# Kernel optimization log

Measured on AMD Instinct MI355X. Metric: run time of the kernel, lower is better.

Reference implementation:

```python
import jax, jax.numpy as jnp
import numpy as np

HIDDEN = 4096
N_HEADS = 32
N_KV_HEADS = 8
D_HEAD = HIDDEN // N_HEADS  # 128
SEQ_LEN = 2048
ROPE_THETA = 10000.0


def _rope(t, start_index):
    # t: [L, n_heads, d_head]; rotate-half (Llama-style) RoPE
    L, _, d = t.shape
    inv_freq = 1.0 / (ROPE_THETA ** (jnp.arange(0, d, 2, dtype=jnp.float32) / d))  # [d/2]
    pos = jnp.arange(L, dtype=jnp.float32) + jnp.float32(start_index)  # [L]
    ang = pos[:, None] * inv_freq  # [L, d/2]
    cos = jnp.cos(ang)[:, None, :].astype(t.dtype)  # [L, 1, d/2]
    sin = jnp.sin(ang)[:, None, :].astype(t.dtype)
    t1, t2 = jnp.split(t, 2, axis=-1)
    return jnp.concatenate([t1 * cos - t2 * sin, t1 * sin + t2 * cos], axis=-1)


def setup_inputs() -> dict:
    key = jax.random.key(0)
    ks = jax.random.split(key, 5)
    s = 1.0 / np.sqrt(HIDDEN)
    return {
        "x": jax.random.normal(ks[0], (SEQ_LEN, HIDDEN), dtype=jnp.float32),
        "Wq": jax.random.normal(ks[1], (HIDDEN, N_HEADS * D_HEAD), dtype=jnp.float32) * s,
        "Wk": jax.random.normal(ks[2], (HIDDEN, N_KV_HEADS * D_HEAD), dtype=jnp.float32) * s,
        "Wv": jax.random.normal(ks[3], (HIDDEN, N_KV_HEADS * D_HEAD), dtype=jnp.float32) * s,
        "Wo": jax.random.normal(ks[4], (N_HEADS * D_HEAD, HIDDEN), dtype=jnp.float32) * s,
        "start_index": 0,
    }


def reference(x, Wq, Wk, Wv, Wo, start_index):
    # x: [L, hidden]; start_index==0 -> cache reset, so post-write cache == current k, v
    L, _ = x.shape
    q = (x @ Wq).reshape(L, N_HEADS, D_HEAD)
    k = (x @ Wk).reshape(L, N_KV_HEADS, D_HEAD)
    v = (x @ Wv).reshape(L, N_KV_HEADS, D_HEAD)
    q = _rope(q, start_index)
    k = _rope(k, start_index)
    # KV cache read: full cache is just [L] entries (prefill)
    S = L
    g = N_HEADS // N_KV_HEADS
    qh = q.transpose(1, 0, 2).reshape(N_KV_HEADS, g, L, D_HEAD)  # [kv, g, L, d]
    kh = k.transpose(1, 0, 2)  # [kv, S, d]
    vh = v.transpose(1, 0, 2)  # [kv, S, d]
    scale = 1.0 / np.sqrt(D_HEAD)
    scores = jnp.einsum('kgld,ksd->kgls', qh, kh) * jnp.asarray(scale, qh.dtype)
    # is_causal = (L > 1): tril(L, S) mask
    causal = jnp.tril(jnp.ones((L, S), dtype=bool))
    neg = jnp.asarray(jnp.finfo(scores.dtype).min, scores.dtype)
    scores = jnp.where(causal, scores, neg)
    attn = jax.nn.softmax(scores, axis=-1)
    out = jnp.einsum('kgls,ksd->kgld', attn, vh)  # [kv, g, L, d]
    out = out.reshape(N_HEADS, L, D_HEAD).transpose(1, 0, 2).reshape(L, N_HEADS * D_HEAD)
    return out @ Wo
```

## Files before the change

kernel.cpp:

```cpp
#include <hip/hip_runtime.h>

typedef unsigned short u16;
typedef float f32x4 __attribute__((ext_vector_type(4)));
typedef __bf16 bf16x8 __attribute__((ext_vector_type(8)));
typedef u16 u16x8 __attribute__((ext_vector_type(8)));

#define VMCNT(n) asm volatile("s_waitcnt vmcnt(" #n ")" ::: "memory")

static __device__ __forceinline__ u16 f2bf(float f) {
  union { float f; unsigned u; } v; v.f = f;
  unsigned r = v.u + 0x7fffu + ((v.u >> 16) & 1u);
  return (u16)(r >> 16);
}
static __device__ __forceinline__ u16 f2bf_n(float f) {
  __bf16 h = (__bf16)f;
  return __builtin_bit_cast(u16, h);
}
static __device__ __forceinline__ float bf2f(u16 x) {
  union { unsigned u; float f; } v; v.u = (unsigned)x << 16; return v.f;
}

static __device__ __forceinline__ f32x4 mfma16(u16x8 a, u16x8 b, f32x4 c) {
  return __builtin_amdgcn_mfma_f32_16x16x32_bf16(
      __builtin_bit_cast(bf16x8, a), __builtin_bit_cast(bf16x8, b), c, 0, 0, 0);
}

static __device__ __forceinline__ void load_lds16(const void* g, void* l) {
  __builtin_amdgcn_global_load_lds(
      (const __attribute__((address_space(1))) void*)g,
      (__attribute__((address_space(3))) void*)l, 16, 0, 0);
}

__global__ void cvt_f32_bf16_swz(const float* __restrict__ in, u16* __restrict__ out, int n8) {
  int i = blockIdx.x * blockDim.x + threadIdx.x;
  if (i >= n8) return;
  int row = i >> 9;
  int j = i & 511;
  int jp = (j & ~7) | ((j & 7) ^ (row & 7));
  const float* src = in + (size_t)i * 8;
  u16x8 o;
  #pragma unroll
  for (int e = 0; e < 8; e++) o[e] = f2bf(src[e]);
  *(u16x8*)(out + ((size_t)row << 12) + jp * 8) = o;
}

__global__ __launch_bounds__(256)
void transpose_cvt(const float* __restrict__ W, u16* __restrict__ Wt, int K, int N) {
  __shared__ float tile[128][33];
  const int k0 = blockIdx.x * 128, n0 = blockIdx.y * 32;
  const int tr = threadIdx.x >> 3;
  const int tc4 = (threadIdx.x & 7) * 4;
  #pragma unroll
  for (int it = 0; it < 4; it++) {
    int kl = it * 32 + tr;
    float4 v = *(const float4*)&W[(size_t)(k0 + kl) * N + n0 + tc4];
    tile[kl][tc4] = v.x; tile[kl][tc4 + 1] = v.y;
    tile[kl][tc4 + 2] = v.z; tile[kl][tc4 + 3] = v.w;
  }
  __syncthreads();
  const int nl = threadIdx.x >> 4;
  const int dch = threadIdx.x & 15;
  #pragma unroll
  for (int it = 0; it < 2; it++) {
    int n = n0 + it * 16 + nl;
    int sch = (dch & 8) | ((dch & 7) ^ (n & 7));
    u16x8 o;
    #pragma unroll
    for (int e = 0; e < 8; e++) o[e] = f2bf(tile[sch * 8 + e][it * 16 + nl]);
    *(u16x8*)&Wt[(size_t)n * K + k0 + dch * 8] = o;
  }
}

__global__ __launch_bounds__(256)
void transpose_cvt2(const float* __restrict__ Wk, const float* __restrict__ Wv,
                    u16* __restrict__ Wkt, u16* __restrict__ Wvt, int K, int N) {
  __shared__ float tile[128][33];
  const int sel = blockIdx.y >= (unsigned)(N / 32);
  const int n0 = (blockIdx.y - (sel ? N / 32 : 0)) * 32;
  const float* W = sel ? Wv : Wk;
  u16* Wt = sel ? Wvt : Wkt;
  const int k0 = blockIdx.x * 128;
  const int tr = threadIdx.x >> 3;
  const int tc4 = (threadIdx.x & 7) * 4;
  #pragma unroll
  for (int it = 0; it < 4; it++) {
    int kl = it * 32 + tr;
    float4 v = *(const float4*)&W[(size_t)(k0 + kl) * N + n0 + tc4];
    tile[kl][tc4] = v.x; tile[kl][tc4 + 1] = v.y;
    tile[kl][tc4 + 2] = v.z; tile[kl][tc4 + 3] = v.w;
  }
  __syncthreads();
  const int nl = threadIdx.x >> 4;
  const int dch = threadIdx.x & 15;
  #pragma unroll
  for (int it = 0; it < 2; it++) {
    int n = n0 + it * 16 + nl;
    int sch = (dch & 8) | ((dch & 7) ^ (n & 7));
    u16x8 o;
    #pragma unroll
    for (int e = 0; e < 8; e++) o[e] = f2bf(tile[sch * 8 + e][it * 16 + nl]);
    *(u16x8*)&Wt[(size_t)n * K + k0 + dch * 8] = o;
  }
}

__global__ __launch_bounds__(256)
void vtrans_k(const u16* __restrict__ qkv, u16* __restrict__ vt) {
  __shared__ u16 tile[32][33];
  int tx = threadIdx.x & 31, ty = threadIdx.x >> 5;
  int s0 = blockIdx.x * 32;
  int d0 = (blockIdx.y & 3) * 32;
  int hk = blockIdx.y >> 2;
  const u16* src = qkv + 5120 + (size_t)hk * 128;
  #pragma unroll
  for (int i = ty; i < 32; i += 8)
    tile[i][tx] = src[(size_t)(s0 + i) * 6144 + d0 + tx];
  __syncthreads();
  u16* dst = vt + (size_t)hk * 128 * 2048;
  #pragma unroll
  for (int i = ty; i < 32; i += 8) {
    int d = d0 + i;
    int s = s0 + tx;
    int sw = (s & ~63) | ((((s >> 3) & 7) ^ (d & 7)) << 3) | (s & 7);
    dst[(size_t)d * 2048 + sw] = tile[tx][i];
  }
}

__global__ void rope_table_k(float2* __restrict__ tab, const int* __restrict__ start, int L) {
  int i = blockIdx.x * blockDim.x + threadIdx.x;
  if (i >= L * 64) return;
  int p = i >> 6, j = i & 63;
  float inv = powf(10000.0f, -(float)j / 64.0f);
  float ang = (float)(p + start[0]) * inv;
  tab[i] = make_float2(cosf(ang), sinf(ang));
}

__global__ void rope_apply_b(const u16* __restrict__ in, int istride, int icol,
                             u16* __restrict__ outp, const float2* __restrict__ tab,
                             int total, int H, float scale, int swz) {
  int i = blockIdx.x * blockDim.x + threadIdx.x;
  if (i >= total) return;
  int j8 = (i & 7) * 8;
  int h = (i >> 3) % H;
  int p = i / (8 * H);
  const u16* base = in + (size_t)p * istride + icol + h * 128;
  u16x8 a = *(const u16x8*)(base + j8);
  u16x8 b = *(const u16x8*)(base + j8 + 64);
  u16x8 o1, o2;
  #pragma unroll
  for (int e = 0; e < 8; e++) {
    float2 cs = tab[p * 64 + j8 + e];
    float av = bf2f(a[e]), bv = bf2f(b[e]);
    o1[e] = f2bf((av * cs.x - bv * cs.y) * scale);
    o2[e] = f2bf((av * cs.y + bv * cs.x) * scale);
  }
  int c1 = i & 7;
  int cs1 = swz ? (c1 ^ (p & 7)) : c1;
  u16* ob = outp + ((size_t)p * H + h) * 128 + cs1 * 8;
  *(u16x8*)ob = o1;
  *(u16x8*)(ob + 64) = o2;
}

template<int BN, bool OUT_BF16>
__global__ __launch_bounds__(256, 2)
void gemm8p(const u16* __restrict__ A, const u16* __restrict__ Bt,
            float* __restrict__ Cf, u16* __restrict__ Cb, int N, int K, int gm) {
  constexpr int N_REP = BN / 32;
  constexpr int NHALF = N_REP / 2;
  __shared__ alignas(16) u16 As[2][128 * 64];
  __shared__ alignas(16) u16 Bs[2][BN * 64];
  const int tid = threadIdx.x;
  const int lane = tid & 63;
  const int wid = tid >> 6;
  const int ql = lane & 15, kg = lane >> 4;
  const int wr = wid >> 1, wcn = wid & 1;

  const int nb = gridDim.x;
  const int b = blockIdx.x;
  const int swz = (b & 7) * (nb >> 3) + (b >> 3);
  const int m0 = (swz % gm) * 128;
  const int n0 = (swz / gm) * BN;

  const int srow = tid >> 3, schk = tid & 7;
  const u16* abase = A + (size_t)(m0 + srow) * K + schk * 8;
  const u16* bbase = Bt + (size_t)(n0 + srow) * K + schk * 8;

  auto stA = [&](int buf, int t, int c) {
    load_lds16(abase + (size_t)(c * 32) * K + t * 64,
               &As[buf][((c * 32 + srow) * 8 + schk) * 8]);
  };
  auto stB = [&](int buf, int t, int c) {
    load_lds16(bbase + (size_t)(c * 32) * K + t * 64,
               &Bs[buf][((c * 32 + srow) * 8 + schk) * 8]);
  };

  f32x4 acc[4][N_REP] = {};
  u16x8 af[2][2];
  u16x8 bfr[NHALF][2];
  u16x8 bpre[NHALF][2];
  const int NT = K / 64;

  stA(0, 0, 0); stA(0, 0, 1); stA(0, 0, 2); stA(0, 0, 3);
  #pragma unroll
  for (int c = 0; c < BN / 32; c++) stB(0, 0, c);
  VMCNT(0);
  __builtin_amdgcn_sched_barrier(0);
  __builtin_amdgcn_s_barrier();
  #pragma unroll
  for (int ni = 0; ni < NHALF; ni++)
    #pragma unroll
    for (int kk = 0; kk < 2; kk++) {
      int R = wcn * (16 * N_REP) + ni * 16 + ql;
      int ch = ((kk << 2) | kg) ^ (ql & 7);
      bpre[ni][kk] = *(const u16x8*)&Bs[0][(R * 8 + ch) * 8];
    }

  #pragma unroll 1
  for (int i = 0; i < NT / 2; i++) {
    const bool tail = (i == NT / 2 - 1);
    #pragma unroll
    for (int p = 0; p < 8; p++) {
      const int q = p & 3;
      const int m = q >> 1, n2 = q & 1;
      const int cbuf = (p < 4) ? 0 : 1;
      if (q == 0 || q == 2) {
        #pragma unroll
        for (int mi = 0; mi < 2; mi++)
          #pragma unroll
          for (int kk = 0; kk < 2; kk++) {
            int row = wr * 64 + m * 32 + mi * 16 + ql;
            int ch = ((kk << 2) | kg) ^ (ql & 7);
            af[mi][kk] = *(const u16x8*)&As[cbuf][(row * 8 + ch) * 8];
          }
      }
      if (q == 1) {
        #pragma unroll
        for (int ni = 0; ni < NHALF; ni++)
          #pragma unroll
          for (int kk = 0; kk < 2; kk++) {
            int R = wcn * (16 * N_REP) + 16 * NHALF + ni * 16 + ql;
            int ch = ((kk << 2) | kg) ^ (ql & 7);
            bfr[ni][kk] = *(const u16x8*)&Bs[cbuf][(R * 8 + ch) * 8];
          }
      }
      const int st = 2 * i + 1 + (p >= 4 ? 1 : 0);
      const int sbuf = st & 1;
      if (st < NT) {
        if constexpr (BN == 192) {
          if (q == 0) { stA(sbuf, st, 0); stA(sbuf, st, 2); stB(sbuf, st, 0); }
          else if (q == 1) { stB(sbuf, st, 1); stB(sbuf, st, 3); stB(sbuf, st, 4); }
          else if (q == 2) { stB(sbuf, st, 2); stB(sbuf, st, 5); }
          else { stA(sbuf, st, 1); stA(sbuf, st, 3); }
        } else {
          if (q == 0) { stA(sbuf, st, 0); stA(sbuf, st, 2); stB(sbuf, st, 0); }
          else if (q == 1) { stB(sbuf, st, 2); stB(sbuf, st, 1); }
          else if (q == 2) { stB(sbuf, st, 3); }
          else { stA(sbuf, st, 1); stA(sbuf, st, 3); }
        }
      }
      if (!tail || p < 4) {
        if constexpr (BN == 192) {
          if (q == 1) VMCNT(6);
          else if (q == 3) VMCNT(4);
          else VMCNT(5);
        } else {
          if (q == 0 || q == 1) VMCNT(5);
          else VMCNT(3);
        }
      } else {
        if (p == 4) VMCNT(2);
        else VMCNT(0);
      }
      __builtin_amdgcn_sched_barrier(0);
      __builtin_amdgcn_s_barrier();
      asm volatile("s_waitcnt lgkmcnt(0)" ::: "memory");
      __builtin_amdgcn_sched_barrier(0);
      if (q == 3) {
        const int nbuf = (p == 3) ? 1 : 0;
        const bool valid = (p == 3) || (2 * i + 2 < NT);
        if (valid) {
          #pragma unroll
          for (int ni = 0; ni < NHALF; ni++)
            #pragma unroll
            for (int kk = 0; kk < 2; kk++) {
              int R = wcn * (16 * N_REP) + ni * 16 + ql;
              int ch = ((kk << 2) | kg) ^ (ql & 7);
              bpre[ni][kk] = *(const u16x8*)&Bs[nbuf][(R * 8 + ch) * 8];
            }
        }
      }
      __builtin_amdgcn_s_setprio(1);
      #pragma unroll
      for (int mi = 0; mi < 2; mi++)
        #pragma unroll
        for (int ni = 0; ni < NHALF; ni++)
          #pragma unroll
          for (int kk = 0; kk < 2; kk++) {
            if (n2 == 0)
              acc[m * 2 + mi][ni] = mfma16(af[mi][kk], bpre[ni][kk], acc[m * 2 + mi][ni]);
            else
              acc[m * 2 + mi][NHALF + ni] = mfma16(af[mi][kk], bfr[ni][kk], acc[m * 2 + mi][NHALF + ni]);
          }
      __builtin_amdgcn_s_setprio(0);
      __builtin_amdgcn_sched_barrier(0);
      __builtin_amdgcn_s_barrier();
    }
  }

  #pragma unroll
  for (int a = 0; a < 4; a++) {
    #pragma unroll
    for (int j = 0; j < N_REP; j++) {
      int row0 = m0 + wr * 64 + (a >> 1) * 32 + (a & 1) * 16 + kg * 4;
      int col = n0 + wcn * (16 * N_REP) + j * 16 + ql;
      #pragma unroll
      for (int r = 0; r < 4; r++) {
        if constexpr (OUT_BF16)
          Cb[(size_t)(row0 + r) * N + col] = f2bf(acc[a][j][r]);
        else
          Cf[(size_t)(row0 + r) * N + col] = acc[a][j][r];
      }
    }
  }
}

__global__ __launch_bounds__(256, 2)
void attn_k(const u16* __restrict__ qkv, const u16* __restrict__ kr,
            const u16* __restrict__ vt, const float2* __restrict__ tab,
            u16* __restrict__ out, float qscale) {
  __shared__ alignas(16) u16 Kls[2][64 * 128];
  __shared__ alignas(16) u16 Vls[2][128 * 64];
  __shared__ alignas(16) u16 Plds[4][16][72];
  const int tid = threadIdx.x;
  const int lane = tid & 63, wave = tid >> 6;
  const int ql = lane & 15, kg = lane >> 4;

  const int b = blockIdx.x;
  const int bswz = (b & 7) * 64 + (b >> 3);
  const int h = bswz >> 4;
  const int bxx = bswz & 15;
  const int hk = h >> 2;

  const u16* kbase = kr + (size_t)hk * 128 + (size_t)(tid >> 4) * 1024 + (tid & 15) * 8;
  const u16* vbase = vt + (size_t)hk * 128 * 2048 + (size_t)(tid >> 3) * 2048 + (tid & 7) * 8;

  int cur = 0;
  #pragma unroll 1
  for (int half_idx = 0; half_idx < 2; half_idx++) {
    const int tile = half_idx ? (31 - bxx) : bxx;
    const int q0 = tile * 64;
    const int qw = q0 + wave * 16;
    const int nsteps = tile + 1;

    u16x8 qf[4];
    {
      const u16* qsrc = qkv + (size_t)(qw + ql) * 6144 + h * 128;
      u16x8 qa[4];
      #pragma unroll
      for (int kk = 0; kk < 4; kk++)
        qa[kk] = *(const u16x8*)(qsrc + kk * 32 + kg * 8);
      const float2* trow = tab + (size_t)(qw + ql) * 64;
      #pragma unroll
      for (int pr = 0; pr < 2; pr++) {
        #pragma unroll
        for (int e = 0; e < 8; e++) {
          float2 cs = trow[pr * 32 + kg * 8 + e];
          float a = bf2f(qa[pr][e]);
          float bb = bf2f(qa[pr + 2][e]);
          qf[pr][e]     = f2bf((a * cs.x - bb * cs.y) * qscale);
          qf[pr + 2][e] = f2bf((a * cs.y + bb * cs.x) * qscale);
        }
      }
    }

    f32x4 acc[8] = {};
    float m_run = -3e38f, l_run = 0.f;

    __syncthreads();
    cur = 0;
    #pragma unroll
    for (int r = 0; r < 4; r++)
      load_lds16(kbase + (size_t)r * 16 * 1024, &Kls[0][(r * 256 + tid) * 8]);
    #pragma unroll
    for (int r = 0; r < 4; r++)
      load_lds16(vbase + (size_t)r * 32 * 2048, &Vls[0][(r * 256 + tid) * 8]);

    #pragma unroll 1
    for (int t = 0; t < nsteps; t++) {
      const int s0 = t * 64;
      const bool last = (t == nsteps - 1);
      __syncthreads();
      if (t + 1 < nsteps) {
        const u16* kn = kbase + (size_t)(s0 + 64) * 1024;
        #pragma unroll
        for (int r = 0; r < 4; r++)
          load_lds16(kn + (size_t)r * 16 * 1024, &Kls[cur ^ 1][(r * 256 + tid) * 8]);
        const u16* vn = vbase + (s0 + 64);
        #pragma unroll
        for (int r = 0; r < 4; r++)
          load_lds16(vn + (size_t)r * 32 * 2048, &Vls[cur ^ 1][(r * 256 + tid) * 8]);
      }
      f32x4 sc[4] = {};
      __builtin_amdgcn_s_setprio(1);
      #pragma unroll
      for (int sb = 0; sb < 4; sb++) {
        const u16* krow = &Kls[cur][(sb * 16 + ql) * 128];
        #pragma unroll
        for (int kk = 0; kk < 4; kk++) {
          u16x8 kf = *(const u16x8*)(krow + (((kk * 4 + kg) ^ (ql & 7)) * 8));
          sc[sb] = mfma16(kf, qf[kk], sc[sb]);
        }
      }
      __builtin_amdgcn_s_setprio(0);
      float mt;
      if (last) {
        const int qg = qw + ql;
        mt = -3e38f;
        #pragma unroll
        for (int sb = 0; sb < 4; sb++)
          #pragma unroll
          for (int r = 0; r < 4; r++) {
            int s = s0 + sb * 16 + kg * 4 + r;
            float v = (s > qg) ? -3e38f : sc[sb][r];
            sc[sb][r] = v;
            mt = fmaxf(mt, v);
          }
      } else {
        float a0 = fmaxf(sc[0][0], sc[0][1]), a1 = fmaxf(sc[0][2], sc[0][3]);
        float a2 = fmaxf(sc[1][0], sc[1][1]), a3 = fmaxf(sc[1][2], sc[1][3]);
        float a4 = fmaxf(sc[2][0], sc[2][1]), a5 = fmaxf(sc[2][2], sc[2][3]);
        float a6 = fmaxf(sc[3][0], sc[3][1]), a7 = fmaxf(sc[3][2], sc[3][3]);
        float b0 = fmaxf(a0, a1), b1 = fmaxf(a2, a3);
        float b2 = fmaxf(a4, a5), b3 = fmaxf(a6, a7);
        mt = fmaxf(fmaxf(b0, b1), fmaxf(b2, b3));
      }
      mt = fmaxf(mt, __shfl_xor(mt, 16, 64));
      mt = fmaxf(mt, __shfl_xor(mt, 32, 64));
      if (!__all(mt - m_run <= 11.5f)) {
        float m_new = fmaxf(m_run, mt);
        float fco = exp2f(m_run - m_new);
        float fr[4];
        #pragma unroll
        for (int r = 0; r < 4; r++) fr[r] = __shfl(fco, (lane & 48) | (kg * 4 + r), 64);
        #pragma unroll
        for (int db = 0; db < 8; db++)
          #pragma unroll
          for (int r = 0; r < 4; r++) acc[db][r] *= fr[r];
        l_run *= fco;
        m_run = m_new;
      }
      float rs = 0.f;
      #pragma unroll
      for (int sb = 0; sb < 4; sb++) {
        float e0 = exp2f(sc[sb][0] - m_run);
        float e1 = exp2f(sc[sb][1] - m_run);
        float e2 = exp2f(sc[sb][2] - m_run);
        float e3 = exp2f(sc[sb][3] - m_run);
        rs += (e0 + e1) + (e2 + e3);
        ushort4 pk;
        pk.x = f2bf_n(e0); pk.y = f2bf_n(e1);
        pk.z = f2bf_n(e2); pk.w = f2bf_n(e3);
        *(ushort4*)&Plds[wave][ql][sb * 16 + kg * 4] = pk;
      }
      rs += __shfl_xor(rs, 16, 64);
      rs += __shfl_xor(rs, 32, 64);
      l_run += rs;
      __builtin_amdgcn_s_setprio(1);
      #pragma unroll
      for (int hf = 0; hf < 2; hf++) {
        u16x8 pf = *(const u16x8*)&Plds[wave][ql][hf * 32 + kg * 8];
        #pragma unroll
        for (int db = 0; db < 8; db++) {
          u16x8 vf = *(const u16x8*)&Vls[cur][((db * 16 + ql) << 6) +
                                              (((hf * 4 + kg) ^ (ql & 7)) << 3)];
          acc[db] = mfma16(pf, vf, acc[db]);
        }
      }
      __builtin_amdgcn_s_setprio(0);
      cur ^= 1;
    }

    float linv[4];
    #pragma unroll
    for (int r = 0; r < 4; r++)
      linv[r] = 1.f / __shfl(l_run, (lane & 48) | (kg * 4 + r), 64);
    #pragma unroll
    for (int db = 0; db < 8; db++) {
      int d = db * 16 + ql;
      #pragma unroll
      for (int r = 0; r < 4; r++) {
        int q = qw + kg * 4 + r;
        int col = (h * 128 + d) ^ ((q & 7) << 3);
        out[(size_t)q * 4096 + col] = f2bf_n(acc[db][r] * linv[r]);
      }
    }
  }
}

extern "C" void kernel_launch(void* const* d_in, const int* in_sizes, int n_in,
                              void* d_out, int out_size, void* d_ws, size_t ws_size,
                              hipStream_t stream) {
  const float* x  = (const float*)d_in[0];
  const float* Wq = (const float*)d_in[1];
  const float* Wk = (const float*)d_in[2];
  const float* Wv = (const float*)d_in[3];
  const float* Wo = (const float*)d_in[4];
  const int* start = (const int*)d_in[5];

  const int L = 2048, HID = 4096, NH = 32, NKV = 8;
  const int NQ = 4096, NKVD = 1024, NF = 6144;

  char* ws = (char*)d_ws;
  size_t off = 0;
  auto alloc = [&](size_t bytes) {
    void* p = ws + off;
    off += (bytes + 255) & ~(size_t)255;
    return p;
  };
  u16* x_b   = (u16*)alloc((size_t)L * HID * 2);
  u16* Wq_t  = (u16*)alloc((size_t)NQ * HID * 2);
  u16* Wk_t  = (u16*)alloc((size_t)NKVD * HID * 2);
  u16* Wv_t  = (u16*)alloc((size_t)NKVD * HID * 2);
  u16* Wo_t  = (u16*)alloc((size_t)HID * NQ * 2);
  u16* k_r   = (u16*)alloc((size_t)L * NKVD * 2);
  u16* vt_b  = (u16*)alloc((size_t)NKV * 128 * L * 2);
  float2* tab = (float2*)alloc((size_t)L * 64 * sizeof(float2));
  u16* qkv_b  = (u16*)d_out;
  u16* attn_b = Wq_t;

  const float qscale = 0.08838834764831845f * 1.4426950408889634f;

  cvt_f32_bf16_swz<<<(L * HID / 8 + 255) / 256, 256, 0, stream>>>(x, x_b, L * HID / 8);
  transpose_cvt<<<dim3(HID / 128, NQ / 32), 256, 0, stream>>>(Wq, Wq_t, HID, NQ);
  transpose_cvt2<<<dim3(HID / 128, 2 * NKVD / 32), 256, 0, stream>>>(Wk, Wv, Wk_t, Wv_t, HID, NKVD);
  transpose_cvt<<<dim3(NQ / 128, HID / 32), 256, 0, stream>>>(Wo, Wo_t, NQ, HID);
  rope_table_k<<<(L * 64 + 255) / 256, 256, 0, stream>>>(tab, start, L);

  gemm8p<192, true><<<512, 256, 0, stream>>>(x_b, Wq_t, nullptr, qkv_b, NF, HID, 16);

  rope_apply_b<<<(L * NKV * 8 + 255) / 256, 256, 0, stream>>>(qkv_b, NF, NQ, k_r, tab, L * NKV * 8, NKV, 1.0f, 1);
  vtrans_k<<<dim3(L / 32, 32), 256, 0, stream>>>(qkv_b, vt_b);

  attn_k<<<512, 256, 0, stream>>>(qkv_b, k_r, vt_b, tab, attn_b, qscale);

  gemm8p<128, false><<<512, 256, 0, stream>>>(attn_b, Wo_t, (float*)d_out, nullptr, HID, NQ, 16);
}
```

Baseline: 310.0 us.

## Simplify GEMM pipeline to four phases with whole-tile staging

Replaces the 8-phase GEMM main loop with a 4-phase loop. The old loop interleaved fine-grained global-to-LDS stages with tuned vmcnt waits and split B fragments into prefetched halves. The new loop issues each next K-tile as one bulk stage, loads all B fragments at once per buffer, and waits with vmcnt(0) every other phase. This needs fewer barriers and less bookkeeping, but the coarser waits reduce overlap between memory loads and MFMA work, and holding all B fragments raises register use.

```diff
diff --git a/kernel.cpp b/kernel.cpp
--- a/kernel.cpp
+++ b/kernel.cpp
@@ -162,10 +162,9 @@
 
 template<int BN, bool OUT_BF16>
 __global__ __launch_bounds__(256, 2)
-void gemm8p(const u16* __restrict__ A, const u16* __restrict__ Bt,
+void gemm4p(const u16* __restrict__ A, const u16* __restrict__ Bt,
             float* __restrict__ Cf, u16* __restrict__ Cb, int N, int K, int gm) {
   constexpr int N_REP = BN / 32;
-  constexpr int NHALF = N_REP / 2;
   __shared__ alignas(16) u16 As[2][128 * 64];
   __shared__ alignas(16) u16 Bs[2][BN * 64];
   const int tid = threadIdx.x;
@@ -192,114 +191,64 @@
     load_lds16(bbase + (size_t)(c * 32) * K + t * 64,
                &Bs[buf][((c * 32 + srow) * 8 + schk) * 8]);
   };
+  auto stageAll = [&](int buf, int t) {
+    stA(buf, t, 0); stA(buf, t, 1); stA(buf, t, 2); stA(buf, t, 3);
+    #pragma unroll
+    for (int c = 0; c < N_REP; c++) stB(buf, t, c);
+  };
 
   f32x4 acc[4][N_REP] = {};
   u16x8 af[2][2];
-  u16x8 bfr[NHALF][2];
-  u16x8 bpre[NHALF][2];
+  u16x8 bfull[N_REP][2];
   const int NT = K / 64;
 
-  stA(0, 0, 0); stA(0, 0, 1); stA(0, 0, 2); stA(0, 0, 3);
-  #pragma unroll
-  for (int c = 0; c < BN / 32; c++) stB(0, 0, c);
+  stageAll(0, 0);
   VMCNT(0);
   __builtin_amdgcn_sched_barrier(0);
   __builtin_amdgcn_s_barrier();
-  #pragma unroll
-  for (int ni = 0; ni < NHALF; ni++)
-    #pragma unroll
-    for (int kk = 0; kk < 2; kk++) {
-      int R = wcn * (16 * N_REP) + ni * 16 + ql;
-      int ch = ((kk << 2) | kg) ^ (ql & 7);
-      bpre[ni][kk] = *(const u16x8*)&Bs[0][(R * 8 + ch) * 8];
-    }
 
   #pragma unroll 1
   for (int i = 0; i < NT / 2; i++) {
-    const bool tail = (i == NT / 2 - 1);
-    #pragma unroll
-    for (int p = 0; p < 8; p++) {
-      const int q = p & 3;
-      const int m = q >> 1, n2 = q & 1;
-      const int cbuf = (p < 4) ? 0 : 1;
-      if (q == 0 || q == 2) {
-        #pragma unroll
-        for (int mi = 0; mi < 2; mi++)
+    #pragma unroll
+    for (int p = 0; p < 4; p++) {
+      const int mh = p & 1;
+      const int cbuf = p >> 1;
+      #pragma unroll
+      for (int mi = 0; mi < 2; mi++)
+        #pragma unroll
+        for (int kk = 0; kk < 2; kk++) {
+          int row = wr * 64 + mh * 32 + mi * 16 + ql;
+          int ch = ((kk << 2) | kg) ^ (ql & 7);
+          af[mi][kk] = *(const u16x8*)&As[cbuf][(row * 8 + ch) * 8];
+        }
+      if (mh == 0) {
+        #pragma unroll
+        for (int j = 0; j < N_REP; j++)
           #pragma unroll
           for (int kk = 0; kk < 2; kk++) {
-            int row = wr * 64 + m * 32 + mi * 16 + ql;
+            int R = wcn * (16 * N_REP) + j * 16 + ql;
             int ch = ((kk << 2) | kg) ^ (ql & 7);
-            af[mi][kk] = *(const u16x8*)&As[cbuf][(row * 8 + ch) * 8];
+            bfull[j][kk] = *(const u16x8*)&Bs[cbuf][(R * 8 + ch) * 8];
           }
       }
-      if (q == 1) {
-        #pragma unroll
-        for (int ni = 0; ni < NHALF; ni++)
-          #pragma unroll
-          for (int kk = 0; kk < 2; kk++) {
-            int R = wcn * (16 * N_REP) + 16 * NHALF + ni * 16 + ql;
-            int ch = ((kk << 2) | kg) ^ (ql & 7);
-            bfr[ni][kk] = *(const u16x8*)&Bs[cbuf][(R * 8 + ch) * 8];
-          }
-      }
-      const int st = 2 * i + 1 + (p >= 4 ? 1 : 0);
-      const int sbuf = st & 1;
-      if (st < NT) {
-        if constexpr (BN == 192) {
-          if (q == 0) { stA(sbuf, st, 0); stA(sbuf, st, 2); stB(sbuf, st, 0); }
-          else if (q == 1) { stB(sbuf, st, 1); stB(sbuf, st, 3); stB(sbuf, st, 4); }
-          else if (q == 2) { stB(sbuf, st, 2); stB(sbuf, st, 5); }
-          else { stA(sbuf, st, 1); stA(sbuf, st, 3); }
-        } else {
-          if (q == 0) { stA(sbuf, st, 0); stA(sbuf, st, 2); stB(sbuf, st, 0); }
-          else if (q == 1) { stB(sbuf, st, 2); stB(sbuf, st, 1); }
-          else if (q == 2) { stB(sbuf, st, 3); }
-          else { stA(sbuf, st, 1); stA(sbuf, st, 3); }
-        }
-      }
-      if (!tail || p < 4) {
-        if constexpr (BN == 192) {
-          if (q == 1) VMCNT(6);
-          else if (q == 3) VMCNT(4);
-          else VMCNT(5);
-        } else {
-          if (q == 0 || q == 1) VMCNT(5);
-          else VMCNT(3);
-        }
-      } else {
-        if (p == 4) VMCNT(2);
-        else VMCNT(0);
-      }
+      if (p == 0) {
+        stageAll(1, 2 * i + 1);
+      } else if (p == 2) {
+        if (2 * i + 2 < NT) stageAll(0, 2 * i + 2);
+      }
+      if (mh == 1) VMCNT(0);
       __builtin_amdgcn_sched_barrier(0);
       __builtin_amdgcn_s_barrier();
       asm volatile("s_waitcnt lgkmcnt(0)" ::: "memory");
       __builtin_amdgcn_sched_barrier(0);
-      if (q == 3) {
-        const int nbuf = (p == 3) ? 1 : 0;
-        const bool valid = (p == 3) || (2 * i + 2 < NT);
-        if (valid) {
+      __builtin_amdgcn_s_setprio(1);
+      #pragma unroll
+      for (int mi = 0; mi < 2; mi++)
+        #pragma unroll
+        for (int j = 0; j < N_REP; j++)
           #pragma unroll
-          for (int ni = 0; ni < NHALF; ni++)
-            #pragma unroll
-            for (int kk = 0; kk < 2; kk++) {
-              int R = wcn * (16 * N_REP) + ni * 16 + ql;
-              int ch = ((kk << 2) | kg) ^ (ql & 7);
-              bpre[ni][kk] = *(const u16x8*)&Bs[nbuf][(R * 8 + ch) * 8];
-            }
-        }
-      }
-      __builtin_amdgcn_s_setprio(1);
-      #pragma unroll
-      for (int mi = 0; mi < 2; mi++)
-        #pragma unroll
-        for (int ni = 0; ni < NHALF; ni++)
-          #pragma unroll
-          for (int kk = 0; kk < 2; kk++) {
-            if (n2 == 0)
-              acc[m * 2 + mi][ni] = mfma16(af[mi][kk], bpre[ni][kk], acc[m * 2 + mi][ni]);
-            else
-              acc[m * 2 + mi][NHALF + ni] = mfma16(af[mi][kk], bfr[ni][kk], acc[m * 2 + mi][NHALF + ni]);
-          }
+          for (int kk = 0; kk < 2; kk++)
+            acc[mh * 2 + mi][j] = mfma16(af[mi][kk], bfull[j][kk], acc[mh * 2 + mi][j]);
       __builtin_amdgcn_s_setprio(0);
       __builtin_amdgcn_sched_barrier(0);
       __builtin_amdgcn_s_barrier();
@@ -535,12 +484,12 @@
   transpose_cvt<<<dim3(NQ / 128, HID / 32), 256, 0, stream>>>(Wo, Wo_t, NQ, HID);
   rope_table_k<<<(L * 64 + 255) / 256, 256, 0, stream>>>(tab, start, L);
 
-  gemm8p<192, true><<<512, 256, 0, stream>>>(x_b, Wq_t, nullptr, qkv_b, NF, HID, 16);
+  gemm4p<192, true><<<512, 256, 0, stream>>>(x_b, Wq_t, nullptr, qkv_b, NF, HID, 16);
 
   rope_apply_b<<<(L * NKV * 8 + 255) / 256, 256, 0, stream>>>(qkv_b, NF, NQ, k_r, tab, L * NKV * 8, NKV, 1.0f, 1);
   vtrans_k<<<dim3(L / 32, 32), 256, 0, stream>>>(qkv_b, vt_b);
 
   attn_k<<<512, 256, 0, stream>>>(qkv_b, k_r, vt_b, tab, attn_b, qscale);
 
-  gemm8p<128, false><<<512, 256, 0, stream>>>(attn_b, Wo_t, (float*)d_out, nullptr, HID, NQ, 16);
-}
+  gemm4p<128, false><<<512, 256, 0, stream>>>(attn_b, Wo_t, (float*)d_out, nullptr, HID, NQ, 16);
+}
```

Result: no change. 312.1 us (+0.7%).
